# Optimization experiments

Measured on AMD Instinct MI355X. Metric: run time of the kernel, lower is better.

## Reference

```python
import jax, jax.numpy as jnp
import numpy as np

N = 100000   # skill_num
D = 128      # skill_embed_dim
E = 500000   # edges per relation
S = 16384    # queried skills
NEG_SLOPE = 0.2


def _gat(x, edge_index, W, att_src, att_dst, bias):
    # PyG GATConv, heads=1, add_self_loops=True, eval mode (no dropout)
    n = x.shape[0]
    loops = jnp.arange(n)
    src = jnp.concatenate([edge_index[0], loops])
    dst = jnp.concatenate([edge_index[1], loops])
    h = x @ W                              # [N, D]
    a_src = h @ att_src                    # [N]
    a_dst = h @ att_dst                    # [N]
    e = jax.nn.leaky_relu(a_src[src] + a_dst[dst], NEG_SLOPE)  # [E+N]
    emax = jax.ops.segment_max(e, dst, num_segments=n)
    ex = jnp.exp(e - emax[dst])
    denom = jax.ops.segment_sum(ex, dst, num_segments=n)
    alpha = ex / (denom[dst] + 1e-16)
    out = jax.ops.segment_sum(alpha[:, None] * h[src], dst, num_segments=n)
    return out + bias


def _sage(x, edge_index, Wl, bl, Wr):
    # PyG SAGEConv, aggr='mean', root_weight=True (lin_r has no bias)
    n = x.shape[0]
    src, dst = edge_index[0], edge_index[1]
    ones = jnp.ones((src.shape[0],), dtype=x.dtype)
    deg = jax.ops.segment_sum(ones, dst, num_segments=n)
    agg = jax.ops.segment_sum(x[src], dst, num_segments=n)
    agg = agg / jnp.maximum(deg, 1.0)[:, None]
    return agg @ Wl + bl + x @ Wr


def setup_inputs() -> dict:
    key = jax.random.key(0)
    ks = jax.random.split(key, 16)
    sc = 1.0 / np.sqrt(D)
    inp = {
        "s": jax.random.randint(ks[0], (S,), 0, N),
        "t_s": 0,
        "t_e": 12,
        "ei_parent": jax.random.randint(ks[1], (2, E), 0, N),
        "ei_child": jax.random.randint(ks[2], (2, E), 0, N),
        "ei_relate": jax.random.randint(ks[3], (2, E), 0, N),
        "emb": jax.random.normal(ks[4], (N, D), dtype=jnp.float32),
        # GAT is_parent params
        "Wp": jax.random.normal(ks[5], (D, D), dtype=jnp.float32) * sc,
        "asp": jax.random.normal(ks[6], (D,), dtype=jnp.float32) * sc,
        "adp": jax.random.normal(ks[7], (D,), dtype=jnp.float32) * sc,
        "bp": jnp.zeros((D,), dtype=jnp.float32),
        # GAT is_child params
        "Wc": jax.random.normal(ks[8], (D, D), dtype=jnp.float32) * sc,
        "asc": jax.random.normal(ks[9], (D,), dtype=jnp.float32) * sc,
        "adc": jax.random.normal(ks[10], (D,), dtype=jnp.float32) * sc,
        "bc": jnp.zeros((D,), dtype=jnp.float32),
        # SAGE relate params
        "Wl": jax.random.normal(ks[11], (D, D), dtype=jnp.float32) * sc,
        "bl": jnp.zeros((D,), dtype=jnp.float32),
        "Wr": jax.random.normal(ks[12], (D, D), dtype=jnp.float32) * sc,
    }
    return inp


def reference(s, t_s, t_e, ei_parent, ei_child, ei_relate, emb,
              Wp, asp, adp, bp, Wc, asc, adc, bc, Wl, bl, Wr):
    out_parent = _gat(emb, ei_parent, Wp, asp, adp, bp)
    out_child = _gat(emb, ei_child, Wc, asc, adc, bc)
    out_relate = _sage(emb, ei_relate, Wl, bl, Wr)
    # HeteroConv(aggr='mean') over the three relation outputs
    node_out = (out_parent + out_child + out_relate) / 3.0
    return node_out[s, :]
```

## Files before the change

kernel.cpp:

```cpp
#include <hip/hip_runtime.h>

#define D 128
#define CAP 64
#define OVF_CAP 1024

typedef short bf16x8 __attribute__((ext_vector_type(8)));
typedef float f32x4 __attribute__((ext_vector_type(4)));

__device__ __forceinline__ unsigned short f2bf(float f) {
  unsigned u = __builtin_bit_cast(unsigned, f);
  unsigned r = (u + 0x7fffu + ((u >> 16) & 1u)) >> 16;
  return (unsigned short)r;
}
__device__ __forceinline__ float bflo(unsigned r) {
  return __builtin_bit_cast(float, r << 16);
}
__device__ __forceinline__ float bfhi(unsigned r) {
  return __builtin_bit_cast(float, r & 0xffff0000u);
}
__device__ __forceinline__ float lrelu(float t) {
  return t >= 0.f ? t : 0.2f * t;
}
__device__ __forceinline__ int swz(int b) { return b ^ (((b >> 8) & 7) << 4); }


__global__ void k_setup(const float* __restrict__ Wp, const float* __restrict__ asp,
                        const float* __restrict__ adp, const float* __restrict__ Wc,
                        const float* __restrict__ asc, const float* __restrict__ adc,
                        const float* __restrict__ bp, const float* __restrict__ bc,
                        const float* __restrict__ bl, const float* __restrict__ Wl,
                        const float* __restrict__ Wr,
                        float* __restrict__ v, unsigned short* __restrict__ wpack,
                        int* __restrict__ qid, int* __restrict__ counters,
                        int* __restrict__ deg5, int N, int S5) {
  int i = blockIdx.x * blockDim.x + threadIdx.x;
  int stride = gridDim.x * blockDim.x;
  for (int k = i; k < N; k += stride) qid[k] = -1;
  for (int k = i; k < S5; k += stride) deg5[k] = 0;
  if (i < 16) counters[i] = 0;

  for (int idx = i; idx < 16 * 8 * 64 * 8; idx += stride) {
    int j    = idx & 7;
    int lane = (idx >> 3) & 63;
    int nt   = (idx >> 9) & 7;
    int kt   = idx >> 12;
    int o = kt >> 2;
    int c = (kt & 3) * 32 + (lane >> 4) * 8 + j;
    int n = nt * 16 + (lane & 15);
    const float* W = (o == 0) ? Wp : (o == 1) ? Wc : (o == 2) ? Wl : Wr;
    wpack[idx] = f2bf(W[c * D + n]);
  }

  if (blockIdx.x == 0) {
    int hw = threadIdx.x >> 5;
    int ln = threadIdx.x & 31;
    float4 as4p = ((const float4*)asp)[ln];
    float4 ad4p = ((const float4*)adp)[ln];
    float4 as4c = ((const float4*)asc)[ln];
    float4 ad4c = ((const float4*)adc)[ln];
    for (int k = hw; k < D; k += 8) {
      float4 wp4 = ((const float4*)(Wp + (size_t)k * D))[ln];
      float4 wc4 = ((const float4*)(Wc + (size_t)k * D))[ln];
      float s0 = wp4.x * as4p.x + wp4.y * as4p.y + wp4.z * as4p.z + wp4.w * as4p.w;
      float s1 = wp4.x * ad4p.x + wp4.y * ad4p.y + wp4.z * ad4p.z + wp4.w * ad4p.w;
      float s2 = wc4.x * as4c.x + wc4.y * as4c.y + wc4.z * as4c.z + wc4.w * as4c.w;
      float s3 = wc4.x * ad4c.x + wc4.y * ad4c.y + wc4.z * ad4c.z + wc4.w * ad4c.w;
#pragma unroll
      for (int o = 16; o > 0; o >>= 1) {
        s0 += __shfl_down(s0, o, 32);
        s1 += __shfl_down(s1, o, 32);
        s2 += __shfl_down(s2, o, 32);
        s3 += __shfl_down(s3, o, 32);
      }
      if (ln == 0) {
        v[k] = s0; v[D + k] = s1; v[2 * D + k] = s2; v[3 * D + k] = s3;
      }
    }
    if (threadIdx.x < D) {
      int k = threadIdx.x;
      v[4 * D + k] = bp[k] + bc[k] + bl[k];
    }
  }
}

__global__ void k_pre(const int* __restrict__ s, int* __restrict__ qid,
                      int* __restrict__ uniq, int* __restrict__ counters, int S,
                      const float* __restrict__ emb, const float* __restrict__ v,
                      float* __restrict__ a_sp, float* __restrict__ a_dp,
                      float* __restrict__ a_sc, float* __restrict__ a_dc,
                      float* __restrict__ selfP, float* __restrict__ selfC,
                      unsigned* __restrict__ ebf, int N) {
  int gtid = blockIdx.x * blockDim.x + threadIdx.x;
  int lane = threadIdx.x & 63;
  if (gtid < S) {
    int n = s[gtid];
    bool won = (atomicCAS(&qid[n], -1, -2) == -1);
    unsigned long long mask = __ballot(won);
    if (mask != 0ull) {
      int leader = __builtin_ctzll(mask);
      int base = 0;
      if (lane == leader) base = atomicAdd(&counters[0], __popcll(mask));
      base = __shfl(base, leader);
      if (won) {
        int u = base + __popcll(mask & ((1ull << lane) - 1ull));
        uniq[u] = n;
        qid[n] = u;
      }
    }
  }
  int node = (gtid >> 6) * 2 + (lane >> 5);
  int c = lane & 31;
  if (node >= N) return;
  float4 x4 = ((const float4*)(emb + (size_t)node * D))[c];
  uint2 p;
  p.x = ((unsigned)f2bf(x4.x)) | (((unsigned)f2bf(x4.y)) << 16);
  p.y = ((unsigned)f2bf(x4.z)) | (((unsigned)f2bf(x4.w)) << 16);
  ((uint2*)ebf)[(size_t)node * 32 + c] = p;
  float4 v0 = ((const float4*)(v))[c];
  float4 v1 = ((const float4*)(v + D))[c];
  float4 v2 = ((const float4*)(v + 2 * D))[c];
  float4 v3 = ((const float4*)(v + 3 * D))[c];
  float s0 = x4.x * v0.x + x4.y * v0.y + x4.z * v0.z + x4.w * v0.w;
  float s1 = x4.x * v1.x + x4.y * v1.y + x4.z * v1.z + x4.w * v1.w;
  float s2 = x4.x * v2.x + x4.y * v2.y + x4.z * v2.z + x4.w * v2.w;
  float s3 = x4.x * v3.x + x4.y * v3.y + x4.z * v3.z + x4.w * v3.w;
#pragma unroll
  for (int o = 16; o > 0; o >>= 1) {
    s0 += __shfl_down(s0, o);
    s1 += __shfl_down(s1, o);
    s2 += __shfl_down(s2, o);
    s3 += __shfl_down(s3, o);
  }
  if (c == 0) {
    a_sp[node] = s0; a_dp[node] = s1; a_sc[node] = s2; a_dc[node] = s3;
    selfP[node] = __expf(lrelu(s0 + s1));
    selfC[node] = __expf(lrelu(s2 + s3));
  }
}

__global__ void __launch_bounds__(256) k_filter(
    const int* __restrict__ eiP, const int* __restrict__ eiC,
    const int* __restrict__ eiR, const int* __restrict__ qid,
    int2* __restrict__ bktP, int2* __restrict__ bktC, int* __restrict__ bktR,
    int* __restrict__ degP, int* __restrict__ degC, int* __restrict__ degR,
    float* __restrict__ denP, float* __restrict__ denC,
    const float* __restrict__ a_sp, const float* __restrict__ a_dp,
    const float* __restrict__ a_sc, const float* __restrict__ a_dc,
    int2* __restrict__ ovf, int* __restrict__ counters, int E) {
  int rel = blockIdx.y;
  const int* ei = (rel == 0) ? eiP : (rel == 1) ? eiC : eiR;
  int e = blockIdx.x * 256 + threadIdx.x;
  if (e >= E) return;
  int dst = ei[E + e];
  int u = qid[dst];
  if (u < 0) return;
  int src = ei[e];
  int* deg = (rel == 0) ? degP : (rel == 1) ? degC : degR;
  int pos = atomicAdd(&deg[u], 1);
  if (rel == 2) {
    if (pos < CAP) {
      bktR[u * CAP + pos] = src;
    } else {
      int o = atomicAdd(&counters[6], 1);
      if (o < OVF_CAP) { int2 tt; tt.x = src; tt.y = u; ovf[2 * OVF_CAP + o] = tt; }
    }
  } else {
    const float* a_s = (rel == 0) ? a_sp : a_sc;
    const float* a_d = (rel == 0) ? a_dp : a_dc;
    float wgt = __expf(lrelu(a_s[src] + a_d[dst]));
    atomicAdd((rel == 0) ? &denP[u] : &denC[u], wgt);
    if (pos < CAP) {
      int2 tt; tt.x = src; tt.y = __builtin_bit_cast(int, wgt);
      ((rel == 0) ? bktP : bktC)[u * CAP + pos] = tt;
    } else {
      int o = atomicAdd(&counters[4 + rel], 1);
      if (o < OVF_CAP) { int2 tt; tt.x = src; tt.y = u; ovf[rel * OVF_CAP + o] = tt; }
    }
  }
}

__global__ void __launch_bounds__(512) k_fused(
    const int2* __restrict__ bktP, const int2* __restrict__ bktC,
    const int* __restrict__ bktR,
    const int* __restrict__ degP, const int* __restrict__ degC,
    const int* __restrict__ degR,
    const float* __restrict__ denP, const float* __restrict__ denC,
    const float* __restrict__ a_sp, const float* __restrict__ a_dp,
    const float* __restrict__ a_sc, const float* __restrict__ a_dc,
    const float* __restrict__ selfP, const float* __restrict__ selfC,
    const unsigned* __restrict__ ebf, const float* __restrict__ emb,
    const int* __restrict__ uniq, const int* __restrict__ counters,
    const int2* __restrict__ ovf, const float* __restrict__ vvec,
    const unsigned short* __restrict__ wpack, float* __restrict__ outU) {
  __shared__ __align__(16) unsigned short A_lds[16 * 64 * 8];
  int U = counters[0];
  int u0 = blockIdx.x * 16;
  if (u0 >= U) return;
  int tid = threadIdx.x;
  int w = tid >> 6;
  int lane = tid & 63;

  int Lc[3];
#pragma unroll
  for (int r = 0; r < 3; ++r) {
    int L = counters[4 + r];
    Lc[r] = (L > OVF_CAP) ? OVF_CAP : L;
  }

#pragma unroll
  for (int t = 0; t < 2; ++t) {
    int m = 2 * w + t;
    int u = u0 + m;
    float2 z[4];
    if (u < U) {
      int n = uniq[u];
      float2 x2 = ((const float2*)(emb + (size_t)n * D))[lane];
#pragma unroll
      for (int r = 0; r < 3; ++r) {
        int dg = ((r == 0) ? degP : (r == 1) ? degC : degR)[u];
        int mc = (dg < CAP) ? dg : CAP;
        int srcl = 0;
        float wl = 0.f;
        if (r < 2) {
          if (lane < mc) {
            int2 sw_ = ((r == 0) ? bktP : bktC)[u * CAP + lane];
            srcl = sw_.x;
            wl = __builtin_bit_cast(float, sw_.y);
          }
        } else {
          if (lane < mc) { srcl = bktR[u * CAP + lane]; wl = 1.f; }
        }
        float2 a; a.x = 0.f; a.y = 0.f;
        int i = 0;
        for (; i + 4 <= mc; i += 4) {
          int s0 = __shfl(srcl, i),     s1 = __shfl(srcl, i + 1);
          int s2 = __shfl(srcl, i + 2), s3 = __shfl(srcl, i + 3);
          float w0 = __shfl(wl, i),     w1 = __shfl(wl, i + 1);
          float w2 = __shfl(wl, i + 2), w3 = __shfl(wl, i + 3);
          unsigned r0 = ebf[(size_t)s0 * 64 + lane];
          unsigned r1 = ebf[(size_t)s1 * 64 + lane];
          unsigned r2 = ebf[(size_t)s2 * 64 + lane];
          unsigned r3 = ebf[(size_t)s3 * 64 + lane];
          a.x += w0 * bflo(r0) + w1 * bflo(r1) + w2 * bflo(r2) + w3 * bflo(r3);
          a.y += w0 * bfhi(r0) + w1 * bfhi(r1) + w2 * bfhi(r2) + w3 * bfhi(r3);
        }
        for (; i < mc; ++i) {
          int si = __shfl(srcl, i);
          float wi = __shfl(wl, i);
          unsigned rr = ebf[(size_t)si * 64 + lane];
          a.x += wi * bflo(rr);
          a.y += wi * bfhi(rr);
        }
        if (dg > CAP) {
          const float* a_s = (r == 0) ? a_sp : a_sc;
          float adn = (r == 0) ? a_dp[n] : (r == 1) ? a_dc[n] : 0.f;
          for (int l = 0; l < Lc[r]; ++l) {
            int2 ov = ovf[r * OVF_CAP + l];
            if (ov.y == u) {
              float wv = 1.f;
              if (r < 2) wv = __expf(lrelu(a_s[ov.x] + adn));
              unsigned rr = ebf[(size_t)ov.x * 64 + lane];
              a.x += wv * bflo(rr);
              a.y += wv * bfhi(rr);
            }
          }
        }
        if (r == 2) {
          float dgc = (float)dg; if (dgc < 1.f) dgc = 1.f;
          float rc = 1.f / dgc;
          a.x *= rc; a.y *= rc;
        }
        z[r] = a;
      }
      float wP = selfP[n];
      float rP = 1.f / (denP[u] + wP);
      float wC = selfC[n];
      float rC = 1.f / (denC[u] + wC);
      z[0].x = (z[0].x + wP * x2.x) * rP; z[0].y = (z[0].y + wP * x2.y) * rP;
      z[1].x = (z[1].x + wC * x2.x) * rC; z[1].y = (z[1].y + wC * x2.y) * rC;
      z[3] = x2;
    } else {
      z[0].x = 0.f; z[0].y = 0.f; z[1] = z[0]; z[2] = z[0]; z[3] = z[0];
    }
    int ktc = lane >> 4;
    int q = (lane >> 2) & 3;
    int j0 = 2 * (lane & 3);
#pragma unroll
    for (int o = 0; o < 4; ++o) {
      int kt = o * 4 + ktc;
      unsigned pk = ((unsigned)f2bf(z[o].x)) | (((unsigned)f2bf(z[o].y)) << 16);
      int off = ((kt * 64 + q * 16 + m) * 8 + j0) * 2;
      *(unsigned*)((char*)A_lds + swz(off)) = pk;
    }
  }
  __syncthreads();

  f32x4 acc = {0.f, 0.f, 0.f, 0.f};
  const bf16x8* wp = (const bf16x8*)wpack;
#pragma unroll
  for (int kt = 0; kt < 16; ++kt) {
    bf16x8 a = *(const bf16x8*)((const char*)A_lds + swz((kt * 64 + lane) * 16));
    bf16x8 b = wp[(kt * 8 + w) * 64 + lane];
    acc = __builtin_amdgcn_mfma_f32_16x16x32_bf16(a, b, acc, 0, 0, 0);
  }

  int col = w * 16 + (lane & 15);
  int r0 = (lane >> 4) * 4;
  float bv = vvec[4 * D + col] * (1.f / 3.f);
#pragma unroll
  for (int reg = 0; reg < 4; ++reg) {
    int u = u0 + r0 + reg;
    if (u < U) outU[(size_t)u * D + col] = acc[reg] * (1.f / 3.f) + bv;
  }
}

__global__ void k_gather(const int* __restrict__ s, const int* __restrict__ qid,
                         const float4* __restrict__ outU4, float4* __restrict__ out4,
                         int S) {
  int idx = blockIdx.x * blockDim.x + threadIdx.x;
  if (idx >= S * 32) return;
  int i = idx >> 5;
  int c = idx & 31;
  int u = qid[s[i]];
  out4[idx] = outU4[(size_t)u * 32 + c];
}


extern "C" void kernel_launch(void* const* d_in, const int* in_sizes, int n_in,
                              void* d_out, int out_size, void* d_ws, size_t ws_size,
                              hipStream_t stream) {
  const int*   s   = (const int*)d_in[0];
  const int*   eip = (const int*)d_in[3];
  const int*   eic = (const int*)d_in[4];
  const int*   eir = (const int*)d_in[5];
  const float* emb = (const float*)d_in[6];
  const float* Wp  = (const float*)d_in[7];
  const float* asp = (const float*)d_in[8];
  const float* adp = (const float*)d_in[9];
  const float* bp  = (const float*)d_in[10];
  const float* Wc  = (const float*)d_in[11];
  const float* asc = (const float*)d_in[12];
  const float* adc = (const float*)d_in[13];
  const float* bc  = (const float*)d_in[14];
  const float* Wl  = (const float*)d_in[15];
  const float* bl  = (const float*)d_in[16];
  const float* Wr  = (const float*)d_in[17];
  float* out = (float*)d_out;

  const int S = in_sizes[0];
  const int E = in_sizes[3] / 2;
  const int N = in_sizes[6] / D;

  char* base = (char*)d_ws;
  size_t off = 0;
  auto carve = [&](size_t bytes) -> char* {
    char* q = base + off;
    off += (bytes + 255) & ~(size_t)255;
    return q;
  };
  float*    a_sp     = (float*)carve((size_t)N * 4);
  float*    a_dp     = (float*)carve((size_t)N * 4);
  float*    a_sc     = (float*)carve((size_t)N * 4);
  float*    a_dc     = (float*)carve((size_t)N * 4);
  float*    selfP    = (float*)carve((size_t)N * 4);
  float*    selfC    = (float*)carve((size_t)N * 4);
  int*      qid      = (int*)carve((size_t)N * 4);
  unsigned* ebf      = (unsigned*)carve((size_t)N * 64 * 4);
  int*      uniq     = (int*)carve((size_t)S * 4);
  int*      counters = (int*)carve(64);
  float*    vvec     = (float*)carve(5 * D * 4);
  unsigned short* wpack = (unsigned short*)carve((size_t)16 * 8 * 64 * 8 * 2);
  float*    outU     = (float*)carve((size_t)S * D * 4);
  int*      degP     = (int*)carve((size_t)S * 4);
  int*      degC     = (int*)carve((size_t)S * 4);
  int*      degR     = (int*)carve((size_t)S * 4);
  float*    denP     = (float*)carve((size_t)S * 4);
  float*    denC     = (float*)carve((size_t)S * 4);
  int2*     bktP     = (int2*)carve((size_t)S * CAP * 8);
  int2*     bktC     = (int2*)carve((size_t)S * CAP * 8);
  int*      bktR     = (int*)carve((size_t)S * CAP * 4);
  int2*     ovf      = (int2*)carve((size_t)3 * OVF_CAP * 8);
  (void)ws_size; (void)n_in; (void)out_size;

  k_setup<<<256, 256, 0, stream>>>(Wp, asp, adp, Wc, asc, adc, bp, bc, bl, Wl, Wr,
                                   vvec, wpack, qid, counters, degP, N, 5 * S);

  k_pre<<<(N * 32 + 255) / 256, 256, 0, stream>>>(s, qid, uniq, counters, S,
                                                  emb, vvec, a_sp, a_dp, a_sc, a_dc,
                                                  selfP, selfC, ebf, N);

  k_filter<<<dim3((E + 255) / 256, 3), 256, 0, stream>>>(
      eip, eic, eir, qid, bktP, bktC, bktR, degP, degC, degR, denP, denC,
      a_sp, a_dp, a_sc, a_dc, ovf, counters, E);

  k_fused<<<(S + 15) / 16, 512, 0, stream>>>(
      bktP, bktC, bktR, degP, degC, degR, denP, denC,
      a_sp, a_dp, a_sc, a_dc, selfP, selfC, ebf, emb, uniq, counters, ovf,
      vvec, wpack, outU);

  k_gather<<<(S * 32 + 255) / 256, 256, 0, stream>>>(s, qid, (const float4*)outU,
                                                     (float4*)out, S);
}
```

Measured before the change: 202.3 us.

## Merge all five kernels into one cooperative persistent kernel with grid syncs

Replaces the five separate launches (setup, pre, filter, fused, gather) with a single cooperative kernel sized to occupancy times CU count. Stages are separated by grid-wide syncs and use grid-stride loops, which removes per-launch overhead and the gaps between kernels. The previous multi-kernel path is kept as a fallback if the cooperative launch fails. In exchange, grid syncs cost something, the occupancy-limited grid may underfill the irregular stages, and one register budget now covers every stage.

New measurement: 385.8 us. 90.7% more time.

```diff
diff --git a/kernel.cpp b/kernel.cpp
--- a/kernel.cpp
+++ b/kernel.cpp
@@ -1,4 +1,7 @@
 #include <hip/hip_runtime.h>
+#include <hip/hip_cooperative_groups.h>
+
+namespace cg = cooperative_groups;
 
 #define D 128
 #define CAP 64
@@ -22,6 +25,294 @@
   return t >= 0.f ? t : 0.2f * t;
 }
 __device__ __forceinline__ int swz(int b) { return b ^ (((b >> 8) & 7) << 4); }
+
+
+struct Params {
+  const int *s, *eiP, *eiC, *eiR;
+  const float *emb;
+  const float *Wp, *asp, *adp, *bp;
+  const float *Wc, *asc, *adc, *bc;
+  const float *Wl, *bl, *Wr;
+  float *out;
+  float *a_sp, *a_dp, *a_sc, *a_dc, *selfP, *selfC;
+  int *qid;
+  unsigned *ebf;
+  int *uniq, *counters;
+  float *vvec;
+  unsigned short *wpack;
+  float *outU;
+  int *degP, *degC, *degR;
+  float *denP, *denC;
+  int2 *bktP, *bktC;
+  int *bktR;
+  int2 *ovf;
+  int S, E, N;
+};
+
+__global__ void __launch_bounds__(512) k_mega(Params p) {
+  cg::grid_group gg = cg::this_grid();
+  __shared__ __align__(16) unsigned short A_lds[16 * 64 * 8];
+  const int tid = threadIdx.x;
+  const int lane = tid & 63;
+  const int gtid = blockIdx.x * 512 + tid;
+  const int gstride = gridDim.x * 512;
+
+  for (int k = gtid; k < p.N; k += gstride) p.qid[k] = -1;
+  for (int k = gtid; k < 5 * p.S; k += gstride) p.degP[k] = 0;
+  if (gtid < 16) p.counters[gtid] = 0;
+
+  for (int idx = gtid; idx < 16 * 8 * 64 * 8; idx += gstride) {
+    int j   = idx & 7;
+    int ln2 = (idx >> 3) & 63;
+    int nt  = (idx >> 9) & 7;
+    int kt  = idx >> 12;
+    int o = kt >> 2;
+    int c = (kt & 3) * 32 + (ln2 >> 4) * 8 + j;
+    int n = nt * 16 + (ln2 & 15);
+    const float* W = (o == 0) ? p.Wp : (o == 1) ? p.Wc : (o == 2) ? p.Wl : p.Wr;
+    p.wpack[idx] = f2bf(W[c * D + n]);
+  }
+
+  if (gtid < 4096) {
+    int k = gtid >> 5, ln = gtid & 31;
+    float4 as4p = ((const float4*)p.asp)[ln];
+    float4 ad4p = ((const float4*)p.adp)[ln];
+    float4 as4c = ((const float4*)p.asc)[ln];
+    float4 ad4c = ((const float4*)p.adc)[ln];
+    float4 wp4 = ((const float4*)(p.Wp + (size_t)k * D))[ln];
+    float4 wc4 = ((const float4*)(p.Wc + (size_t)k * D))[ln];
+    float s0 = wp4.x * as4p.x + wp4.y * as4p.y + wp4.z * as4p.z + wp4.w * as4p.w;
+    float s1 = wp4.x * ad4p.x + wp4.y * ad4p.y + wp4.z * ad4p.z + wp4.w * ad4p.w;
+    float s2 = wc4.x * as4c.x + wc4.y * as4c.y + wc4.z * as4c.z + wc4.w * as4c.w;
+    float s3 = wc4.x * ad4c.x + wc4.y * ad4c.y + wc4.z * ad4c.z + wc4.w * ad4c.w;
+#pragma unroll
+    for (int o = 16; o > 0; o >>= 1) {
+      s0 += __shfl_down(s0, o, 32);
+      s1 += __shfl_down(s1, o, 32);
+      s2 += __shfl_down(s2, o, 32);
+      s3 += __shfl_down(s3, o, 32);
+    }
+    if (ln == 0) {
+      p.vvec[k] = s0; p.vvec[D + k] = s1;
+      p.vvec[2 * D + k] = s2; p.vvec[3 * D + k] = s3;
+    }
+  } else if (gtid < 4096 + 128) {
+    int k = gtid - 4096;
+    p.vvec[4 * D + k] = p.bp[k] + p.bc[k] + p.bl[k];
+  }
+  gg.sync();
+
+  for (int q = gtid; q < p.S; q += gstride) {
+    int n = p.s[q];
+    bool won = (atomicCAS(&p.qid[n], -1, -2) == -1);
+    unsigned long long mask = __ballot(won);
+    if (mask != 0ull) {
+      int leader = __builtin_ctzll(mask);
+      int base = 0;
+      if (lane == leader) base = atomicAdd(&p.counters[0], __popcll(mask));
+      base = __shfl(base, leader);
+      if (won) {
+        int u = base + __popcll(mask & ((1ull << lane) - 1ull));
+        p.uniq[u] = n;
+        p.qid[n] = u;
+      }
+    }
+  }
+  const int nodeSlots = ((p.N + 1) >> 1) * 64;
+  for (int idx = gtid; idx < nodeSlots; idx += gstride) {
+    int node = (idx >> 6) * 2 + ((idx & 63) >> 5);
+    int c = idx & 31;
+    if (node < p.N) {
+      float4 x4 = ((const float4*)(p.emb + (size_t)node * D))[c];
+      uint2 pk;
+      pk.x = ((unsigned)f2bf(x4.x)) | (((unsigned)f2bf(x4.y)) << 16);
+      pk.y = ((unsigned)f2bf(x4.z)) | (((unsigned)f2bf(x4.w)) << 16);
+      ((uint2*)p.ebf)[(size_t)node * 32 + c] = pk;
+      float4 v0 = ((const float4*)(p.vvec))[c];
+      float4 v1 = ((const float4*)(p.vvec + D))[c];
+      float4 v2 = ((const float4*)(p.vvec + 2 * D))[c];
+      float4 v3 = ((const float4*)(p.vvec + 3 * D))[c];
+      float s0 = x4.x * v0.x + x4.y * v0.y + x4.z * v0.z + x4.w * v0.w;
+      float s1 = x4.x * v1.x + x4.y * v1.y + x4.z * v1.z + x4.w * v1.w;
+      float s2 = x4.x * v2.x + x4.y * v2.y + x4.z * v2.z + x4.w * v2.w;
+      float s3 = x4.x * v3.x + x4.y * v3.y + x4.z * v3.z + x4.w * v3.w;
+#pragma unroll
+      for (int o = 16; o > 0; o >>= 1) {
+        s0 += __shfl_down(s0, o);
+        s1 += __shfl_down(s1, o);
+        s2 += __shfl_down(s2, o);
+        s3 += __shfl_down(s3, o);
+      }
+      if (c == 0) {
+        p.a_sp[node] = s0; p.a_dp[node] = s1;
+        p.a_sc[node] = s2; p.a_dc[node] = s3;
+        p.selfP[node] = __expf(lrelu(s0 + s1));
+        p.selfC[node] = __expf(lrelu(s2 + s3));
+      }
+    }
+  }
+  gg.sync();
+
+  for (int e3 = gtid; e3 < 3 * p.E; e3 += gstride) {
+    int rel = (e3 >= 2 * p.E) ? 2 : (e3 >= p.E) ? 1 : 0;
+    int e = e3 - rel * p.E;
+    const int* ei = (rel == 0) ? p.eiP : (rel == 1) ? p.eiC : p.eiR;
+    int dst = ei[p.E + e];
+    int u = p.qid[dst];
+    if (u < 0) continue;
+    int src = ei[e];
+    int* deg = (rel == 0) ? p.degP : (rel == 1) ? p.degC : p.degR;
+    int pos = atomicAdd(&deg[u], 1);
+    if (rel == 2) {
+      if (pos < CAP) {
+        p.bktR[u * CAP + pos] = src;
+      } else {
+        int o = atomicAdd(&p.counters[6], 1);
+        if (o < OVF_CAP) { int2 tt; tt.x = src; tt.y = u; p.ovf[2 * OVF_CAP + o] = tt; }
+      }
+    } else {
+      const float* a_s = (rel == 0) ? p.a_sp : p.a_sc;
+      const float* a_d = (rel == 0) ? p.a_dp : p.a_dc;
+      float wgt = __expf(lrelu(a_s[src] + a_d[dst]));
+      atomicAdd((rel == 0) ? &p.denP[u] : &p.denC[u], wgt);
+      if (pos < CAP) {
+        int2 tt; tt.x = src; tt.y = __builtin_bit_cast(int, wgt);
+        ((rel == 0) ? p.bktP : p.bktC)[u * CAP + pos] = tt;
+      } else {
+        int o = atomicAdd(&p.counters[4 + rel], 1);
+        if (o < OVF_CAP) { int2 tt; tt.x = src; tt.y = u; p.ovf[rel * OVF_CAP + o] = tt; }
+      }
+    }
+  }
+  gg.sync();
+
+  int U = p.counters[0];
+  int w = tid >> 6;
+  int Lc[3];
+#pragma unroll
+  for (int r = 0; r < 3; ++r) {
+    int L = p.counters[4 + r];
+    Lc[r] = (L > OVF_CAP) ? OVF_CAP : L;
+  }
+
+  for (int tile = blockIdx.x; tile * 16 < U; tile += gridDim.x) {
+    int u0 = tile * 16;
+    __syncthreads();
+#pragma unroll
+    for (int t = 0; t < 2; ++t) {
+      int m = 2 * w + t;
+      int u = u0 + m;
+      float2 z[4];
+      if (u < U) {
+        int n = p.uniq[u];
+        float2 x2 = ((const float2*)(p.emb + (size_t)n * D))[lane];
+#pragma unroll
+        for (int r = 0; r < 3; ++r) {
+          int dg = ((r == 0) ? p.degP : (r == 1) ? p.degC : p.degR)[u];
+          int mc = (dg < CAP) ? dg : CAP;
+          int srcl = 0;
+          float wl = 0.f;
+          if (r < 2) {
+            if (lane < mc) {
+              int2 sw_ = ((r == 0) ? p.bktP : p.bktC)[u * CAP + lane];
+              srcl = sw_.x;
+              wl = __builtin_bit_cast(float, sw_.y);
+            }
+          } else {
+            if (lane < mc) { srcl = p.bktR[u * CAP + lane]; wl = 1.f; }
+          }
+          float2 a; a.x = 0.f; a.y = 0.f;
+          int i = 0;
+          for (; i + 4 <= mc; i += 4) {
+            int s0 = __shfl(srcl, i),     s1 = __shfl(srcl, i + 1);
+            int s2 = __shfl(srcl, i + 2), s3 = __shfl(srcl, i + 3);
+            float w0 = __shfl(wl, i),     w1 = __shfl(wl, i + 1);
+            float w2 = __shfl(wl, i + 2), w3 = __shfl(wl, i + 3);
+            unsigned r0 = p.ebf[(size_t)s0 * 64 + lane];
+            unsigned r1 = p.ebf[(size_t)s1 * 64 + lane];
+            unsigned r2 = p.ebf[(size_t)s2 * 64 + lane];
+            unsigned r3 = p.ebf[(size_t)s3 * 64 + lane];
+            a.x += w0 * bflo(r0) + w1 * bflo(r1) + w2 * bflo(r2) + w3 * bflo(r3);
+            a.y += w0 * bfhi(r0) + w1 * bfhi(r1) + w2 * bfhi(r2) + w3 * bfhi(r3);
+          }
+          for (; i < mc; ++i) {
+            int si = __shfl(srcl, i);
+            float wi = __shfl(wl, i);
+            unsigned rr = p.ebf[(size_t)si * 64 + lane];
+            a.x += wi * bflo(rr);
+            a.y += wi * bfhi(rr);
+          }
+          if (dg > CAP) {
+            const float* a_s = (r == 0) ? p.a_sp : p.a_sc;
+            float adn = (r == 0) ? p.a_dp[n] : (r == 1) ? p.a_dc[n] : 0.f;
+            for (int l = 0; l < Lc[r]; ++l) {
+              int2 ov = p.ovf[r * OVF_CAP + l];
+              if (ov.y == u) {
+                float wv = 1.f;
+                if (r < 2) wv = __expf(lrelu(a_s[ov.x] + adn));
+                unsigned rr = p.ebf[(size_t)ov.x * 64 + lane];
+                a.x += wv * bflo(rr);
+                a.y += wv * bfhi(rr);
+              }
+            }
+          }
+          if (r == 2) {
+            float dgc = (float)dg; if (dgc < 1.f) dgc = 1.f;
+            float rc = 1.f / dgc;
+            a.x *= rc; a.y *= rc;
+          }
+          z[r] = a;
+        }
+        float wP = p.selfP[n];
+        float rP = 1.f / (p.denP[u] + wP);
+        float wC = p.selfC[n];
+        float rC = 1.f / (p.denC[u] + wC);
+        z[0].x = (z[0].x + wP * x2.x) * rP; z[0].y = (z[0].y + wP * x2.y) * rP;
+        z[1].x = (z[1].x + wC * x2.x) * rC; z[1].y = (z[1].y + wC * x2.y) * rC;
+        z[3] = x2;
+      } else {
+        z[0].x = 0.f; z[0].y = 0.f; z[1] = z[0]; z[2] = z[0]; z[3] = z[0];
+      }
+      int ktc = lane >> 4;
+      int q = (lane >> 2) & 3;
+      int j0 = 2 * (lane & 3);
+#pragma unroll
+      for (int o = 0; o < 4; ++o) {
+        int kt = o * 4 + ktc;
+        unsigned pk = ((unsigned)f2bf(z[o].x)) | (((unsigned)f2bf(z[o].y)) << 16);
+        int off = ((kt * 64 + q * 16 + m) * 8 + j0) * 2;
+        *(unsigned*)((char*)A_lds + swz(off)) = pk;
+      }
+    }
+    __syncthreads();
+
+    f32x4 acc = {0.f, 0.f, 0.f, 0.f};
+    const bf16x8* wp = (const bf16x8*)p.wpack;
+#pragma unroll
+    for (int kt = 0; kt < 16; ++kt) {
+      bf16x8 a = *(const bf16x8*)((const char*)A_lds + swz((kt * 64 + lane) * 16));
+      bf16x8 b = wp[(kt * 8 + w) * 64 + lane];
+      acc = __builtin_amdgcn_mfma_f32_16x16x32_bf16(a, b, acc, 0, 0, 0);
+    }
+
+    int col = w * 16 + (lane & 15);
+    int r0 = (lane >> 4) * 4;
+    float bv = p.vvec[4 * D + col] * (1.f / 3.f);
+#pragma unroll
+    for (int reg = 0; reg < 4; ++reg) {
+      int u = u0 + r0 + reg;
+      if (u < U) p.outU[(size_t)u * D + col] = acc[reg] * (1.f / 3.f) + bv;
+    }
+  }
+  gg.sync();
+
+  for (int idx = gtid; idx < p.S * 32; idx += gstride) {
+    int i = idx >> 5;
+    int c = idx & 31;
+    int u = p.qid[p.s[i]];
+    ((float4*)p.out)[idx] = ((const float4*)p.outU)[(size_t)u * 32 + c];
+  }
+}
 
 
 __global__ void k_setup(const float* __restrict__ Wp, const float* __restrict__ asp,
@@ -38,7 +329,6 @@
   for (int k = i; k < N; k += stride) qid[k] = -1;
   for (int k = i; k < S5; k += stride) deg5[k] = 0;
   if (i < 16) counters[i] = 0;
-
   for (int idx = i; idx < 16 * 8 * 64 * 8; idx += stride) {
     int j    = idx & 7;
     int lane = (idx >> 3) & 63;
@@ -50,7 +340,6 @@
     const float* W = (o == 0) ? Wp : (o == 1) ? Wc : (o == 2) ? Wl : Wr;
     wpack[idx] = f2bf(W[c * D + n]);
   }
-
   if (blockIdx.x == 0) {
     int hw = threadIdx.x >> 5;
     int ln = threadIdx.x & 31;
@@ -72,9 +361,7 @@
         s2 += __shfl_down(s2, o, 32);
         s3 += __shfl_down(s3, o, 32);
       }
-      if (ln == 0) {
-        v[k] = s0; v[D + k] = s1; v[2 * D + k] = s2; v[3 * D + k] = s3;
-      }
+      if (ln == 0) { v[k] = s0; v[D + k] = s1; v[2 * D + k] = s2; v[3 * D + k] = s3; }
     }
     if (threadIdx.x < D) {
       int k = threadIdx.x;
@@ -199,14 +486,12 @@
   int tid = threadIdx.x;
   int w = tid >> 6;
   int lane = tid & 63;
-
   int Lc[3];
 #pragma unroll
   for (int r = 0; r < 3; ++r) {
     int L = counters[4 + r];
     Lc[r] = (L > OVF_CAP) ? OVF_CAP : L;
   }
-
 #pragma unroll
   for (int t = 0; t < 2; ++t) {
     int m = 2 * w + t;
@@ -294,7 +579,6 @@
     }
   }
   __syncthreads();
-
   f32x4 acc = {0.f, 0.f, 0.f, 0.f};
   const bf16x8* wp = (const bf16x8*)wpack;
 #pragma unroll
@@ -303,7 +587,6 @@
     bf16x8 b = wp[(kt * 8 + w) * 64 + lane];
     acc = __builtin_amdgcn_mfma_f32_16x16x32_bf16(a, b, acc, 0, 0, 0);
   }
-
   int col = w * 16 + (lane & 15);
   int r0 = (lane >> 4) * 4;
   float bv = vvec[4 * D + col] * (1.f / 3.f);
@@ -382,22 +665,52 @@
   int2*     ovf      = (int2*)carve((size_t)3 * OVF_CAP * 8);
   (void)ws_size; (void)n_in; (void)out_size;
 
-  k_setup<<<256, 256, 0, stream>>>(Wp, asp, adp, Wc, asc, adc, bp, bc, bl, Wl, Wr,
-                                   vvec, wpack, qid, counters, degP, N, 5 * S);
-
-  k_pre<<<(N * 32 + 255) / 256, 256, 0, stream>>>(s, qid, uniq, counters, S,
-                                                  emb, vvec, a_sp, a_dp, a_sc, a_dc,
-                                                  selfP, selfC, ebf, N);
-
-  k_filter<<<dim3((E + 255) / 256, 3), 256, 0, stream>>>(
-      eip, eic, eir, qid, bktP, bktC, bktR, degP, degC, degR, denP, denC,
-      a_sp, a_dp, a_sc, a_dc, ovf, counters, E);
-
-  k_fused<<<(S + 15) / 16, 512, 0, stream>>>(
-      bktP, bktC, bktR, degP, degC, degR, denP, denC,
-      a_sp, a_dp, a_sc, a_dc, selfP, selfC, ebf, emb, uniq, counters, ovf,
-      vvec, wpack, outU);
-
-  k_gather<<<(S * 32 + 255) / 256, 256, 0, stream>>>(s, qid, (const float4*)outU,
-                                                     (float4*)out, S);
-}
+  Params P;
+  P.s = s; P.eiP = eip; P.eiC = eic; P.eiR = eir; P.emb = emb;
+  P.Wp = Wp; P.asp = asp; P.adp = adp; P.bp = bp;
+  P.Wc = Wc; P.asc = asc; P.adc = adc; P.bc = bc;
+  P.Wl = Wl; P.bl = bl; P.Wr = Wr;
+  P.out = out;
+  P.a_sp = a_sp; P.a_dp = a_dp; P.a_sc = a_sc; P.a_dc = a_dc;
+  P.selfP = selfP; P.selfC = selfC;
+  P.qid = qid; P.ebf = ebf; P.uniq = uniq; P.counters = counters;
+  P.vvec = vvec; P.wpack = wpack; P.outU = outU;
+  P.degP = degP; P.degC = degC; P.degR = degR;
+  P.denP = denP; P.denC = denC;
+  P.bktP = bktP; P.bktC = bktC; P.bktR = bktR; P.ovf = ovf;
+  P.S = S; P.E = E; P.N = N;
+
+  static int gridBlocks = 0;
+  if (gridBlocks == 0) {
+    int nb = 0;
+    hipOccupancyMaxActiveBlocksPerMultiprocessor(&nb, k_mega, 512, 0);
+    if (nb < 1) nb = 1;
+    int dev = 0;
+    hipGetDevice(&dev);
+    hipDeviceProp_t prop;
+    int cus = 256;
+    if (hipGetDeviceProperties(&prop, dev) == hipSuccess && prop.multiProcessorCount > 0)
+      cus = prop.multiProcessorCount;
+    gridBlocks = nb * cus;
+  }
+
+  void* args[] = {(void*)&P};
+  hipError_t err = hipLaunchCooperativeKernel(k_mega, dim3(gridBlocks), dim3(512),
+                                              args, 0, stream);
+  if (err != hipSuccess) {
+    k_setup<<<256, 256, 0, stream>>>(Wp, asp, adp, Wc, asc, adc, bp, bc, bl, Wl, Wr,
+                                     vvec, wpack, qid, counters, degP, N, 5 * S);
+    k_pre<<<(N * 32 + 255) / 256, 256, 0, stream>>>(s, qid, uniq, counters, S,
+                                                    emb, vvec, a_sp, a_dp, a_sc, a_dc,
+                                                    selfP, selfC, ebf, N);
+    k_filter<<<dim3((E + 255) / 256, 3), 256, 0, stream>>>(
+        eip, eic, eir, qid, bktP, bktC, bktR, degP, degC, degR, denP, denC,
+        a_sp, a_dp, a_sc, a_dc, ovf, counters, E);
+    k_fused<<<(S + 15) / 16, 512, 0, stream>>>(
+        bktP, bktC, bktR, degP, degC, degR, denP, denC,
+        a_sp, a_dp, a_sc, a_dc, selfP, selfC, ebf, emb, uniq, counters, ovf,
+        vvec, wpack, outU);
+    k_gather<<<(S * 32 + 255) / 256, 256, 0, stream>>>(s, qid, (const float4*)outU,
+                                                       (float4*)out, S);
+  }
+}
```

## Drop bf16 embedding copy and use grid-stride loops with fixed grids

Applied to the files above, without the earlier changes.

Removes the full-table bf16 conversion of the embedding in the precompute kernel, so the aggregation kernel now gathers neighbour rows straight from the fp32 embedding. This saves writing a 25.6 MB bf16 table but doubles the bytes read per gathered neighbour. The precompute, filter and gather kernels also switch to grid-stride loops over fixed grids, and the filter kernel flattens its three relations into one 1D loop. The ballot-based dedup in the precompute kernel now runs inside a loop whose lanes can diverge across iterations.

Result: slower. 209.4 us (+3.5%).

```diff
diff --git a/kernel.cpp b/kernel.cpp
--- a/kernel.cpp
+++ b/kernel.cpp
@@ -11,12 +11,6 @@
   unsigned u = __builtin_bit_cast(unsigned, f);
   unsigned r = (u + 0x7fffu + ((u >> 16) & 1u)) >> 16;
   return (unsigned short)r;
-}
-__device__ __forceinline__ float bflo(unsigned r) {
-  return __builtin_bit_cast(float, r << 16);
-}
-__device__ __forceinline__ float bfhi(unsigned r) {
-  return __builtin_bit_cast(float, r & 0xffff0000u);
 }
 __device__ __forceinline__ float lrelu(float t) {
   return t >= 0.f ? t : 0.2f * t;
@@ -89,11 +83,13 @@
                       float* __restrict__ a_sp, float* __restrict__ a_dp,
                       float* __restrict__ a_sc, float* __restrict__ a_dc,
                       float* __restrict__ selfP, float* __restrict__ selfC,
-                      unsigned* __restrict__ ebf, int N) {
+                      int N) {
   int gtid = blockIdx.x * blockDim.x + threadIdx.x;
+  int gstride = gridDim.x * blockDim.x;
   int lane = threadIdx.x & 63;
-  if (gtid < S) {
-    int n = s[gtid];
+
+  for (int q = gtid; q < S; q += gstride) {
+    int n = s[q];
     bool won = (atomicCAS(&qid[n], -1, -2) == -1);
     unsigned long long mask = __ballot(won);
     if (mask != 0ull) {
@@ -108,33 +104,33 @@
       }
     }
   }
-  int node = (gtid >> 6) * 2 + (lane >> 5);
-  int c = lane & 31;
-  if (node >= N) return;
-  float4 x4 = ((const float4*)(emb + (size_t)node * D))[c];
-  uint2 p;
-  p.x = ((unsigned)f2bf(x4.x)) | (((unsigned)f2bf(x4.y)) << 16);
-  p.y = ((unsigned)f2bf(x4.z)) | (((unsigned)f2bf(x4.w)) << 16);
-  ((uint2*)ebf)[(size_t)node * 32 + c] = p;
-  float4 v0 = ((const float4*)(v))[c];
-  float4 v1 = ((const float4*)(v + D))[c];
-  float4 v2 = ((const float4*)(v + 2 * D))[c];
-  float4 v3 = ((const float4*)(v + 3 * D))[c];
-  float s0 = x4.x * v0.x + x4.y * v0.y + x4.z * v0.z + x4.w * v0.w;
-  float s1 = x4.x * v1.x + x4.y * v1.y + x4.z * v1.z + x4.w * v1.w;
-  float s2 = x4.x * v2.x + x4.y * v2.y + x4.z * v2.z + x4.w * v2.w;
-  float s3 = x4.x * v3.x + x4.y * v3.y + x4.z * v3.z + x4.w * v3.w;
-#pragma unroll
-  for (int o = 16; o > 0; o >>= 1) {
-    s0 += __shfl_down(s0, o);
-    s1 += __shfl_down(s1, o);
-    s2 += __shfl_down(s2, o);
-    s3 += __shfl_down(s3, o);
-  }
-  if (c == 0) {
-    a_sp[node] = s0; a_dp[node] = s1; a_sc[node] = s2; a_dc[node] = s3;
-    selfP[node] = __expf(lrelu(s0 + s1));
-    selfC[node] = __expf(lrelu(s2 + s3));
+
+  const int slots = ((N + 1) >> 1) * 64;
+  for (int idx = gtid; idx < slots; idx += gstride) {
+    int node = (idx >> 6) * 2 + ((idx & 63) >> 5);
+    int c = idx & 31;
+    if (node >= N) continue;
+    float4 x4 = ((const float4*)(emb + (size_t)node * D))[c];
+    float4 v0 = ((const float4*)(v))[c];
+    float4 v1 = ((const float4*)(v + D))[c];
+    float4 v2 = ((const float4*)(v + 2 * D))[c];
+    float4 v3 = ((const float4*)(v + 3 * D))[c];
+    float s0 = x4.x * v0.x + x4.y * v0.y + x4.z * v0.z + x4.w * v0.w;
+    float s1 = x4.x * v1.x + x4.y * v1.y + x4.z * v1.z + x4.w * v1.w;
+    float s2 = x4.x * v2.x + x4.y * v2.y + x4.z * v2.z + x4.w * v2.w;
+    float s3 = x4.x * v3.x + x4.y * v3.y + x4.z * v3.z + x4.w * v3.w;
+#pragma unroll
+    for (int o = 16; o > 0; o >>= 1) {
+      s0 += __shfl_down(s0, o);
+      s1 += __shfl_down(s1, o);
+      s2 += __shfl_down(s2, o);
+      s3 += __shfl_down(s3, o);
+    }
+    if (c == 0) {
+      a_sp[node] = s0; a_dp[node] = s1; a_sc[node] = s2; a_dc[node] = s3;
+      selfP[node] = __expf(lrelu(s0 + s1));
+      selfC[node] = __expf(lrelu(s2 + s3));
+    }
   }
 }
 
@@ -147,34 +143,37 @@
     const float* __restrict__ a_sp, const float* __restrict__ a_dp,
     const float* __restrict__ a_sc, const float* __restrict__ a_dc,
     int2* __restrict__ ovf, int* __restrict__ counters, int E) {
-  int rel = blockIdx.y;
-  const int* ei = (rel == 0) ? eiP : (rel == 1) ? eiC : eiR;
-  int e = blockIdx.x * 256 + threadIdx.x;
-  if (e >= E) return;
-  int dst = ei[E + e];
-  int u = qid[dst];
-  if (u < 0) return;
-  int src = ei[e];
-  int* deg = (rel == 0) ? degP : (rel == 1) ? degC : degR;
-  int pos = atomicAdd(&deg[u], 1);
-  if (rel == 2) {
-    if (pos < CAP) {
-      bktR[u * CAP + pos] = src;
+  int gtid = blockIdx.x * blockDim.x + threadIdx.x;
+  int gstride = gridDim.x * blockDim.x;
+  for (int e3 = gtid; e3 < 3 * E; e3 += gstride) {
+    int rel = (e3 >= 2 * E) ? 2 : (e3 >= E) ? 1 : 0;
+    int e = e3 - rel * E;
+    const int* ei = (rel == 0) ? eiP : (rel == 1) ? eiC : eiR;
+    int dst = ei[E + e];
+    int u = qid[dst];
+    if (u < 0) continue;
+    int src = ei[e];
+    int* deg = (rel == 0) ? degP : (rel == 1) ? degC : degR;
+    int pos = atomicAdd(&deg[u], 1);
+    if (rel == 2) {
+      if (pos < CAP) {
+        bktR[u * CAP + pos] = src;
+      } else {
+        int o = atomicAdd(&counters[6], 1);
+        if (o < OVF_CAP) { int2 tt; tt.x = src; tt.y = u; ovf[2 * OVF_CAP + o] = tt; }
+      }
     } else {
-      int o = atomicAdd(&counters[6], 1);
-      if (o < OVF_CAP) { int2 tt; tt.x = src; tt.y = u; ovf[2 * OVF_CAP + o] = tt; }
-    }
-  } else {
-    const float* a_s = (rel == 0) ? a_sp : a_sc;
-    const float* a_d = (rel == 0) ? a_dp : a_dc;
-    float wgt = __expf(lrelu(a_s[src] + a_d[dst]));
-    atomicAdd((rel == 0) ? &denP[u] : &denC[u], wgt);
-    if (pos < CAP) {
-      int2 tt; tt.x = src; tt.y = __builtin_bit_cast(int, wgt);
-      ((rel == 0) ? bktP : bktC)[u * CAP + pos] = tt;
-    } else {
-      int o = atomicAdd(&counters[4 + rel], 1);
-      if (o < OVF_CAP) { int2 tt; tt.x = src; tt.y = u; ovf[rel * OVF_CAP + o] = tt; }
+      const float* a_s = (rel == 0) ? a_sp : a_sc;
+      const float* a_d = (rel == 0) ? a_dp : a_dc;
+      float wgt = __expf(lrelu(a_s[src] + a_d[dst]));
+      atomicAdd((rel == 0) ? &denP[u] : &denC[u], wgt);
+      if (pos < CAP) {
+        int2 tt; tt.x = src; tt.y = __builtin_bit_cast(int, wgt);
+        ((rel == 0) ? bktP : bktC)[u * CAP + pos] = tt;
+      } else {
+        int o = atomicAdd(&counters[4 + rel], 1);
+        if (o < OVF_CAP) { int2 tt; tt.x = src; tt.y = u; ovf[rel * OVF_CAP + o] = tt; }
+      }
     }
   }
 }
@@ -188,7 +187,7 @@
     const float* __restrict__ a_sp, const float* __restrict__ a_dp,
     const float* __restrict__ a_sc, const float* __restrict__ a_dc,
     const float* __restrict__ selfP, const float* __restrict__ selfC,
-    const unsigned* __restrict__ ebf, const float* __restrict__ emb,
+    const float* __restrict__ emb,
     const int* __restrict__ uniq, const int* __restrict__ counters,
     const int2* __restrict__ ovf, const float* __restrict__ vvec,
     const unsigned short* __restrict__ wpack, float* __restrict__ outU) {
@@ -199,6 +198,7 @@
   int tid = threadIdx.x;
   int w = tid >> 6;
   int lane = tid & 63;
+  const float2* er = (const float2*)emb;
 
   int Lc[3];
 #pragma unroll
@@ -214,7 +214,7 @@
     float2 z[4];
     if (u < U) {
       int n = uniq[u];
-      float2 x2 = ((const float2*)(emb + (size_t)n * D))[lane];
+      float2 x2 = er[(size_t)n * 64 + lane];
 #pragma unroll
       for (int r = 0; r < 3; ++r) {
         int dg = ((r == 0) ? degP : (r == 1) ? degC : degR)[u];
@@ -237,19 +237,19 @@
           int s2 = __shfl(srcl, i + 2), s3 = __shfl(srcl, i + 3);
           float w0 = __shfl(wl, i),     w1 = __shfl(wl, i + 1);
           float w2 = __shfl(wl, i + 2), w3 = __shfl(wl, i + 3);
-          unsigned r0 = ebf[(size_t)s0 * 64 + lane];
-          unsigned r1 = ebf[(size_t)s1 * 64 + lane];
-          unsigned r2 = ebf[(size_t)s2 * 64 + lane];
-          unsigned r3 = ebf[(size_t)s3 * 64 + lane];
-          a.x += w0 * bflo(r0) + w1 * bflo(r1) + w2 * bflo(r2) + w3 * bflo(r3);
-          a.y += w0 * bfhi(r0) + w1 * bfhi(r1) + w2 * bfhi(r2) + w3 * bfhi(r3);
+          float2 r0 = er[(size_t)s0 * 64 + lane];
+          float2 r1 = er[(size_t)s1 * 64 + lane];
+          float2 r2 = er[(size_t)s2 * 64 + lane];
+          float2 r3 = er[(size_t)s3 * 64 + lane];
+          a.x += w0 * r0.x + w1 * r1.x + w2 * r2.x + w3 * r3.x;
+          a.y += w0 * r0.y + w1 * r1.y + w2 * r2.y + w3 * r3.y;
         }
         for (; i < mc; ++i) {
           int si = __shfl(srcl, i);
           float wi = __shfl(wl, i);
-          unsigned rr = ebf[(size_t)si * 64 + lane];
-          a.x += wi * bflo(rr);
-          a.y += wi * bfhi(rr);
+          float2 rr = er[(size_t)si * 64 + lane];
+          a.x += wi * rr.x;
+          a.y += wi * rr.y;
         }
         if (dg > CAP) {
           const float* a_s = (r == 0) ? a_sp : a_sc;
@@ -259,9 +259,9 @@
             if (ov.y == u) {
               float wv = 1.f;
               if (r < 2) wv = __expf(lrelu(a_s[ov.x] + adn));
-              unsigned rr = ebf[(size_t)ov.x * 64 + lane];
-              a.x += wv * bflo(rr);
-              a.y += wv * bfhi(rr);
+              float2 rr = er[(size_t)ov.x * 64 + lane];
+              a.x += wv * rr.x;
+              a.y += wv * rr.y;
             }
           }
         }
@@ -317,12 +317,14 @@
 __global__ void k_gather(const int* __restrict__ s, const int* __restrict__ qid,
                          const float4* __restrict__ outU4, float4* __restrict__ out4,
                          int S) {
-  int idx = blockIdx.x * blockDim.x + threadIdx.x;
-  if (idx >= S * 32) return;
-  int i = idx >> 5;
-  int c = idx & 31;
-  int u = qid[s[i]];
-  out4[idx] = outU4[(size_t)u * 32 + c];
+  int gtid = blockIdx.x * blockDim.x + threadIdx.x;
+  int gstride = gridDim.x * blockDim.x;
+  for (int idx = gtid; idx < S * 32; idx += gstride) {
+    int i = idx >> 5;
+    int c = idx & 31;
+    int u = qid[s[i]];
+    out4[idx] = outU4[(size_t)u * 32 + c];
+  }
 }
 
 
@@ -365,7 +367,6 @@
   float*    selfP    = (float*)carve((size_t)N * 4);
   float*    selfC    = (float*)carve((size_t)N * 4);
   int*      qid      = (int*)carve((size_t)N * 4);
-  unsigned* ebf      = (unsigned*)carve((size_t)N * 64 * 4);
   int*      uniq     = (int*)carve((size_t)S * 4);
   int*      counters = (int*)carve(64);
   float*    vvec     = (float*)carve(5 * D * 4);
@@ -385,19 +386,18 @@
   k_setup<<<256, 256, 0, stream>>>(Wp, asp, adp, Wc, asc, adc, bp, bc, bl, Wl, Wr,
                                    vvec, wpack, qid, counters, degP, N, 5 * S);
 
-  k_pre<<<(N * 32 + 255) / 256, 256, 0, stream>>>(s, qid, uniq, counters, S,
-                                                  emb, vvec, a_sp, a_dp, a_sc, a_dc,
-                                                  selfP, selfC, ebf, N);
-
-  k_filter<<<dim3((E + 255) / 256, 3), 256, 0, stream>>>(
+  k_pre<<<2048, 256, 0, stream>>>(s, qid, uniq, counters, S,
+                                  emb, vvec, a_sp, a_dp, a_sc, a_dc,
+                                  selfP, selfC, N);
+
+  k_filter<<<2048, 256, 0, stream>>>(
       eip, eic, eir, qid, bktP, bktC, bktR, degP, degC, degR, denP, denC,
       a_sp, a_dp, a_sc, a_dc, ovf, counters, E);
 
   k_fused<<<(S + 15) / 16, 512, 0, stream>>>(
       bktP, bktC, bktR, degP, degC, degR, denP, denC,
-      a_sp, a_dp, a_sc, a_dc, selfP, selfC, ebf, emb, uniq, counters, ovf,
+      a_sp, a_dp, a_sc, a_dc, selfP, selfC, emb, uniq, counters, ovf,
       vvec, wpack, outU);
 
-  k_gather<<<(S * 32 + 255) / 256, 256, 0, stream>>>(s, qid, (const float4*)outU,
-                                                     (float4*)out, S);
-}
+  k_gather<<<512, 256, 0, stream>>>(s, qid, (const float4*)outU, (float4*)out, S);
+}
```
